# Optimization experiments

Measured on AMD Instinct MI355X. Metric: run time of the kernel, lower is better.

The kernel has to match this reference:

```python
import jax, jax.numpy as jnp
import numpy as np

N_NODES = 100000
N_EDGES = 1600000
IN_C, HID, OUT_C = 128, 64, 64
N_LAYERS = 16
ALPHA, THETA = 0.1, 0.5


def setup_inputs() -> dict:
    key = jax.random.key(0)
    ks = jax.random.split(key, 8)
    x = jax.random.normal(ks[0], (N_NODES, IN_C), dtype=jnp.float32)
    edge_index = jax.random.randint(ks[1], (2, N_EDGES), 0, N_NODES, dtype=jnp.int64)
    # torch Linear: weight [out, in], bias [out]
    lin0_w = jax.random.normal(ks[2], (HID, IN_C), dtype=jnp.float32) / np.sqrt(IN_C)
    lin0_b = jnp.zeros((HID,), dtype=jnp.float32)
    lin1_w = jax.random.normal(ks[3], (OUT_C, HID), dtype=jnp.float32) / np.sqrt(HID)
    lin1_b = jnp.zeros((OUT_C,), dtype=jnp.float32)
    # GCN2Conv weight1 per layer: [HID, HID], applied as h @ W
    conv_w = jax.random.normal(ks[4], (N_LAYERS, HID, HID), dtype=jnp.float32) / np.sqrt(HID)
    return {"x": x, "edge_index": edge_index, "lin0_w": lin0_w, "lin0_b": lin0_b,
            "lin1_w": lin1_w, "lin1_b": lin1_b, "conv_w": conv_w}


def reference(x, edge_index, lin0_w, lin0_b, lin1_w, lin1_b, conv_w):
    src, dst = edge_index[0], edge_index[1]
    # input projection (dropout p=0 in eval -> identity)
    h = jax.nn.relu(x @ lin0_w.T + lin0_b)  # [N, HID]
    h0 = h
    for l in range(N_LAYERS):
        # unweighted sum aggregation over edges (normalize=False, edge_weight=None)
        agg = jax.ops.segment_sum(h[src], dst, num_segments=N_NODES)  # [N, HID]
        z = (1.0 - ALPHA) * agg + ALPHA * h0  # initial residual
        beta = np.log(THETA / (l + 1) + 1.0).astype(np.float32)  # identity mapping strength
        h = jax.nn.relu((1.0 - beta) * z + beta * (z @ conv_w[l]))
    return h @ lin1_w.T + lin1_b  # [N, OUT_C]
```

## Files before the change

kernel.cpp:

```cpp
#include <hip/hip_runtime.h>
#include <cmath>

#define HID 64
#define IN_C 128

__device__ __forceinline__ float rl(float v, int k) {
    return __uint_as_float(__builtin_amdgcn_readlane(__float_as_uint(v), k));
}
__device__ __forceinline__ float bflo(unsigned u) { return __uint_as_float(u << 16); }
__device__ __forceinline__ float bfhi(unsigned u) { return __uint_as_float(u & 0xffff0000u); }
__device__ __forceinline__ unsigned bfpack(float lo, float hi) {
    unsigned a = __float_as_uint(lo), b = __float_as_uint(hi);
    a = (a + 0x7fffu + ((a >> 16) & 1u)) >> 16;
    b = (b + 0x7fffu + ((b >> 16) & 1u)) & 0xffff0000u;
    return a | b;
}


__global__ void k_hist(const int* __restrict__ dst, int* __restrict__ counts, int E) {
    int e = blockIdx.x * blockDim.x + threadIdx.x;
    if (e < E) atomicAdd(&counts[dst[e]], 1);
}

__global__ void k_scan_block(const int* __restrict__ counts, int* __restrict__ row_ptr,
                             int* __restrict__ chunk_sums, int n) {
    __shared__ int s[1024];
    int i = blockIdx.x * 1024 + threadIdx.x;
    int v = (i < n) ? counts[i] : 0;
    s[threadIdx.x] = v;
    __syncthreads();
    for (int off = 1; off < 1024; off <<= 1) {
        int t = (threadIdx.x >= off) ? s[threadIdx.x - off] : 0;
        __syncthreads();
        s[threadIdx.x] += t;
        __syncthreads();
    }
    if (i < n) row_ptr[i] = s[threadIdx.x] - v;
    if (threadIdx.x == 1023) chunk_sums[blockIdx.x] = s[1023];
}

__global__ void k_scan_fix(int* __restrict__ row_ptr, const int* __restrict__ chunk_sums,
                           int n, int total) {
    __shared__ int base_s;
    if (threadIdx.x == 0) {
        int b = 0;
        for (int c = 0; c < (int)blockIdx.x; ++c) b += chunk_sums[c];
        base_s = b;
    }
    __syncthreads();
    int i = blockIdx.x * 1024 + threadIdx.x;
    if (i < n) row_ptr[i] += base_s;
    if (i == 0) row_ptr[n] = total;
}

__global__ void k_fill(const int* __restrict__ src, const int* __restrict__ dst,
                       const int* __restrict__ row_ptr, int* __restrict__ cursor,
                       int* __restrict__ col_idx, int E) {
    int e = blockIdx.x * blockDim.x + threadIdx.x;
    if (e < E) {
        int d = dst[e];
        int pos = row_ptr[d] + atomicAdd(&cursor[d], 1);
        col_idx[pos] = src[e];
    }
}

__global__ __launch_bounds__(256) void k_lin0(const float* __restrict__ x,
                                              const float* __restrict__ w,
                                              const float* __restrict__ b,
                                              unsigned* __restrict__ h0, int N) {
    __shared__ float Wt[IN_C * 65];
    for (int i = threadIdx.x; i < IN_C * HID; i += 256) {
        int o = i >> 7, k = i & 127;
        Wt[k * 65 + o] = w[i];
    }
    __syncthreads();
    int lane = threadIdx.x & 63;
    int wid = (blockIdx.x * blockDim.x + threadIdx.x) >> 6;
    int nw = (gridDim.x * blockDim.x) >> 6;
    float bias = b[lane];
    for (int n0 = wid; n0 < N; n0 += 2 * nw) {
        int n1 = n0 + nw;
        bool v1 = n1 < N;
        int n1c = v1 ? n1 : n0;
        float xa0 = x[(size_t)n0 * IN_C + lane];
        float xa1 = x[(size_t)n0 * IN_C + 64 + lane];
        float xb0 = x[(size_t)n1c * IN_C + lane];
        float xb1 = x[(size_t)n1c * IN_C + 64 + lane];
        float acc0 = bias, acc1 = bias;
#pragma unroll
        for (int k = 0; k < 64; ++k) {
            float wv = Wt[k * 65 + lane];
            acc0 = fmaf(rl(xa0, k), wv, acc0);
            acc1 = fmaf(rl(xb0, k), wv, acc1);
        }
#pragma unroll
        for (int k = 0; k < 64; ++k) {
            float wv = Wt[(64 + k) * 65 + lane];
            acc0 = fmaf(rl(xa1, k), wv, acc0);
            acc1 = fmaf(rl(xb1, k), wv, acc1);
        }
        acc0 = fmaxf(acc0, 0.f);
        acc1 = fmaxf(acc1, 0.f);
        float p0 = __shfl(acc0, lane | 1);
        float p1 = __shfl(acc1, lane | 1);
        if ((lane & 1) == 0) {
            h0[(size_t)n0 * 32 + (lane >> 1)] = bfpack(acc0, p0);
            if (v1) h0[(size_t)n1 * 32 + (lane >> 1)] = bfpack(acc1, p1);
        }
    }
}

__global__ __launch_bounds__(256) void k_layer(const uint4* __restrict__ hin,
                                               const uint4* __restrict__ h0,
                                               unsigned* __restrict__ hout,
                                               const float* __restrict__ W,
                                               const int* __restrict__ row_ptr,
                                               const int* __restrict__ col_idx,
                                               float beta, int N) {
    __shared__ float Ws[HID * HID];
    for (int i = threadIdx.x; i < HID * HID; i += 256) Ws[i] = W[i];
    __syncthreads();

    int lane = threadIdx.x & 63;
    int sub = lane >> 3;
    int cg = lane & 7;
    int wid = (blockIdx.x * blockDim.x + threadIdx.x) >> 6;
    int nw = (gridDim.x * blockDim.x) >> 6;

    for (int n = wid; n < N; n += nw) {
        int b = row_ptr[n];
        int d = row_ptr[n + 1] - b;
        float a[8];
#pragma unroll
        for (int c = 0; c < 8; ++c) a[c] = 0.f;
        int j = 0;
        for (; j + 16 <= d; j += 16) {
            int i0 = col_idx[b + j + sub];
            int i1 = col_idx[b + j + 8 + sub];
            uint4 q0 = hin[(size_t)i0 * 8 + cg];
            uint4 q1 = hin[(size_t)i1 * 8 + cg];
            a[0] += bflo(q0.x); a[1] += bfhi(q0.x);
            a[2] += bflo(q0.y); a[3] += bfhi(q0.y);
            a[4] += bflo(q0.z); a[5] += bfhi(q0.z);
            a[6] += bflo(q0.w); a[7] += bfhi(q0.w);
            a[0] += bflo(q1.x); a[1] += bfhi(q1.x);
            a[2] += bflo(q1.y); a[3] += bfhi(q1.y);
            a[4] += bflo(q1.z); a[5] += bfhi(q1.z);
            a[6] += bflo(q1.w); a[7] += bfhi(q1.w);
        }
        if (j + sub < d) {
            int i0 = col_idx[b + j + sub];
            uint4 q0 = hin[(size_t)i0 * 8 + cg];
            a[0] += bflo(q0.x); a[1] += bfhi(q0.x);
            a[2] += bflo(q0.y); a[3] += bfhi(q0.y);
            a[4] += bflo(q0.z); a[5] += bfhi(q0.z);
            a[6] += bflo(q0.w); a[7] += bfhi(q0.w);
        }
        if (j + 8 + sub < d) {
            int i1 = col_idx[b + j + 8 + sub];
            uint4 q1 = hin[(size_t)i1 * 8 + cg];
            a[0] += bflo(q1.x); a[1] += bfhi(q1.x);
            a[2] += bflo(q1.y); a[3] += bfhi(q1.y);
            a[4] += bflo(q1.z); a[5] += bfhi(q1.z);
            a[6] += bflo(q1.w); a[7] += bfhi(q1.w);
        }
#pragma unroll
        for (int off = 8; off <= 32; off <<= 1) {
#pragma unroll
            for (int c = 0; c < 8; ++c) a[c] += __shfl_xor(a[c], off);
        }
        uint4 hq = h0[(size_t)n * 8 + cg];
        float z[8];
        z[0] = 0.9f * a[0] + 0.1f * bflo(hq.x);
        z[1] = 0.9f * a[1] + 0.1f * bfhi(hq.x);
        z[2] = 0.9f * a[2] + 0.1f * bflo(hq.y);
        z[3] = 0.9f * a[3] + 0.1f * bfhi(hq.y);
        z[4] = 0.9f * a[4] + 0.1f * bflo(hq.z);
        z[5] = 0.9f * a[5] + 0.1f * bfhi(hq.z);
        z[6] = 0.9f * a[6] + 0.1f * bflo(hq.w);
        z[7] = 0.9f * a[7] + 0.1f * bfhi(hq.w);

        float g = 0.f;
#pragma unroll
        for (int c = 0; c < 8; ++c) {
#pragma unroll
            for (int gg = 0; gg < 8; ++gg) {
                g = fmaf(rl(z[c], gg), Ws[(8 * gg + c) * HID + lane], g);
            }
        }
        int q = lane >> 3;
        float zs[8];
#pragma unroll
        for (int c = 0; c < 8; ++c) zs[c] = __shfl(z[c], q);
        int m = lane & 7;
        float zl = zs[0];
#pragma unroll
        for (int c = 1; c < 8; ++c) zl = (m == c) ? zs[c] : zl;

        float r = fmaxf((1.f - beta) * zl + beta * g, 0.f);
        float rn = __shfl(r, lane | 1);
        if ((lane & 1) == 0) hout[(size_t)n * 32 + (lane >> 1)] = bfpack(r, rn);
    }
}

__global__ __launch_bounds__(256) void k_lin1(const unsigned* __restrict__ h,
                                              const float* __restrict__ w,
                                              const float* __restrict__ b,
                                              float* __restrict__ out, int N) {
    __shared__ float Wt[HID * 65];
    for (int i = threadIdx.x; i < HID * HID; i += 256) {
        int o = i >> 6, k = i & 63;
        Wt[k * 65 + o] = w[i];
    }
    __syncthreads();
    int lane = threadIdx.x & 63;
    int wid = (blockIdx.x * blockDim.x + threadIdx.x) >> 6;
    int nw = (gridDim.x * blockDim.x) >> 6;
    float bias = b[lane];
    for (int n0 = wid; n0 < N; n0 += 2 * nw) {
        int n1 = n0 + nw;
        bool v1 = n1 < N;
        int n1c = v1 ? n1 : n0;
        unsigned ua = h[(size_t)n0 * 32 + (lane >> 1)];
        unsigned ub = h[(size_t)n1c * 32 + (lane >> 1)];
        float ha = (lane & 1) ? bfhi(ua) : bflo(ua);
        float hb = (lane & 1) ? bfhi(ub) : bflo(ub);
        float acc0 = bias, acc1 = bias;
#pragma unroll
        for (int k = 0; k < 64; ++k) {
            float wv = Wt[k * 65 + lane];
            acc0 = fmaf(rl(ha, k), wv, acc0);
            acc1 = fmaf(rl(hb, k), wv, acc1);
        }
        out[(size_t)n0 * HID + lane] = acc0;
        if (v1) out[(size_t)n1 * HID + lane] = acc1;
    }
}

extern "C" void kernel_launch(void* const* d_in, const int* in_sizes, int n_in,
                              void* d_out, int out_size, void* d_ws, size_t ws_size,
                              hipStream_t stream) {
    const float* x      = (const float*)d_in[0];
    const int*   ei     = (const int*)d_in[1];
    const float* lin0_w = (const float*)d_in[2];
    const float* lin0_b = (const float*)d_in[3];
    const float* lin1_w = (const float*)d_in[4];
    const float* lin1_b = (const float*)d_in[5];
    const float* conv_w = (const float*)d_in[6];

    int N = in_sizes[0] / IN_C;
    int E = in_sizes[1] / 2;
    const int* src = ei;
    const int* dst = ei + E;

    unsigned* h0 = (unsigned*)d_ws;
    unsigned* hA = h0 + (size_t)N * 32;
    unsigned* hB = hA + (size_t)N * 32;
    int* row_ptr    = (int*)(hB + (size_t)N * 32);
    int* cursor     = row_ptr + (N + 1);
    int* col_idx    = cursor + N;
    int* chunk_sums = col_idx + E;

    int nch = (N + 1023) / 1024;

    hipMemsetAsync(cursor, 0, (size_t)N * sizeof(int), stream);
    k_hist<<<(E + 255) / 256, 256, 0, stream>>>(dst, cursor, E);
    k_scan_block<<<nch, 1024, 0, stream>>>(cursor, row_ptr, chunk_sums, N);
    k_scan_fix<<<nch, 1024, 0, stream>>>(row_ptr, chunk_sums, N, E);
    hipMemsetAsync(cursor, 0, (size_t)N * sizeof(int), stream);
    k_fill<<<(E + 255) / 256, 256, 0, stream>>>(src, dst, row_ptr, cursor, col_idx, E);

    k_lin0<<<1024, 256, 0, stream>>>(x, lin0_w, lin0_b, h0, N);

    const unsigned* cur = h0;
    for (int l = 0; l < 16; ++l) {
        float beta = (float)log(0.5 / (double)(l + 1) + 1.0);
        unsigned* nxt = (l & 1) ? hB : hA;
        k_layer<<<2048, 256, 0, stream>>>((const uint4*)cur, (const uint4*)h0, nxt,
                                          conv_w + (size_t)l * HID * HID,
                                          row_ptr, col_idx, beta, N);
        cur = nxt;
    }

    k_lin1<<<1024, 256, 0, stream>>>(cur, lin1_w, lin1_b, (float*)d_out, N);
}
```

Baseline: 1.478 ms.

## Use DPP/permlane reductions, bf16-packed LDS weights and LDS z broadcast in layer kernel

After: 1.511 ms. 1.02x slower.

```diff
diff --git a/kernel.cpp b/kernel.cpp
--- a/kernel.cpp
+++ b/kernel.cpp
@@ -14,6 +14,33 @@
     a = (a + 0x7fffu + ((a >> 16) & 1u)) >> 16;
     b = (b + 0x7fffu + ((b >> 16) & 1u)) & 0xffff0000u;
     return a | b;
+}
+
+__device__ __forceinline__ float xadd8(float x) {
+    int t = __builtin_amdgcn_update_dpp(0, __float_as_int(x), 0x128, 0xF, 0xF, true);
+    return x + __int_as_float(t);
+}
+#if __has_builtin(__builtin_amdgcn_permlane16_swap)
+typedef unsigned uvec2 __attribute__((ext_vector_type(2)));
+__device__ __forceinline__ float xadd16(float x) {
+    uvec2 r = __builtin_amdgcn_permlane16_swap(__float_as_uint(x), __float_as_uint(x), false, false);
+    return __uint_as_float(r[0]) + __uint_as_float(r[1]);
+}
+#else
+__device__ __forceinline__ float xadd16(float x) { return x + __shfl_xor(x, 16); }
+#endif
+#if __has_builtin(__builtin_amdgcn_permlane32_swap)
+typedef unsigned uvec2b __attribute__((ext_vector_type(2)));
+__device__ __forceinline__ float xadd32(float x) {
+    uvec2b r = __builtin_amdgcn_permlane32_swap(__float_as_uint(x), __float_as_uint(x), false, false);
+    return __uint_as_float(r[0]) + __uint_as_float(r[1]);
+}
+#else
+__device__ __forceinline__ float xadd32(float x) { return x + __shfl_xor(x, 32); }
+#endif
+__device__ __forceinline__ float pairswap(float x) {
+    int t = __builtin_amdgcn_update_dpp(0, __float_as_int(x), 0xB1, 0xF, 0xF, true);
+    return __int_as_float(t);
 }
 
 
@@ -101,8 +128,8 @@
         }
         acc0 = fmaxf(acc0, 0.f);
         acc1 = fmaxf(acc1, 0.f);
-        float p0 = __shfl(acc0, lane | 1);
-        float p1 = __shfl(acc1, lane | 1);
+        float p0 = pairswap(acc0);
+        float p1 = pairswap(acc1);
         if ((lane & 1) == 0) {
             h0[(size_t)n0 * 32 + (lane >> 1)] = bfpack(acc0, p0);
             if (v1) h0[(size_t)n1 * 32 + (lane >> 1)] = bfpack(acc1, p1);
@@ -117,11 +144,23 @@
                                                const int* __restrict__ row_ptr,
                                                const int* __restrict__ col_idx,
                                                float beta, int N) {
-    __shared__ float Ws[HID * HID];
-    for (int i = threadIdx.x; i < HID * HID; i += 256) Ws[i] = W[i];
+    __shared__ uint2 Wp[16 * 64];
+    __shared__ float zb[4 * 64];
+    for (int idx = threadIdx.x; idx < 16 * 64; idx += 256) {
+        int k4 = idx >> 6, c = idx & 63;
+        float w0 = W[(4 * k4 + 0) * 64 + c];
+        float w1 = W[(4 * k4 + 1) * 64 + c];
+        float w2 = W[(4 * k4 + 2) * 64 + c];
+        float w3 = W[(4 * k4 + 3) * 64 + c];
+        uint2 p;
+        p.x = bfpack(w0, w1);
+        p.y = bfpack(w2, w3);
+        Wp[idx] = p;
+    }
     __syncthreads();
 
     int lane = threadIdx.x & 63;
+    int wslot = threadIdx.x >> 6;
     int sub = lane >> 3;
     int cg = lane & 7;
     int wid = (blockIdx.x * blockDim.x + threadIdx.x) >> 6;
@@ -165,10 +204,12 @@
             a[6] += bflo(q1.w); a[7] += bfhi(q1.w);
         }
 #pragma unroll
-        for (int off = 8; off <= 32; off <<= 1) {
-#pragma unroll
-            for (int c = 0; c < 8; ++c) a[c] += __shfl_xor(a[c], off);
-        }
+        for (int c = 0; c < 8; ++c) a[c] = xadd8(a[c]);
+#pragma unroll
+        for (int c = 0; c < 8; ++c) a[c] = xadd16(a[c]);
+#pragma unroll
+        for (int c = 0; c < 8; ++c) a[c] = xadd32(a[c]);
+
         uint4 hq = h0[(size_t)n * 8 + cg];
         float z[8];
         z[0] = 0.9f * a[0] + 0.1f * bflo(hq.x);
@@ -180,25 +221,28 @@
         z[6] = 0.9f * a[6] + 0.1f * bflo(hq.w);
         z[7] = 0.9f * a[7] + 0.1f * bfhi(hq.w);
 
-        float g = 0.f;
-#pragma unroll
-        for (int c = 0; c < 8; ++c) {
-#pragma unroll
-            for (int gg = 0; gg < 8; ++gg) {
-                g = fmaf(rl(z[c], gg), Ws[(8 * gg + c) * HID + lane], g);
-            }
-        }
-        int q = lane >> 3;
-        float zs[8];
-#pragma unroll
-        for (int c = 0; c < 8; ++c) zs[c] = __shfl(z[c], q);
-        int m = lane & 7;
-        float zl = zs[0];
-#pragma unroll
-        for (int c = 1; c < 8; ++c) zl = (m == c) ? zs[c] : zl;
+        if (sub == 0) {
+            float4 zlo = make_float4(z[0], z[1], z[2], z[3]);
+            float4 zhi = make_float4(z[4], z[5], z[6], z[7]);
+            *(float4*)&zb[wslot * 64 + cg * 8]     = zlo;
+            *(float4*)&zb[wslot * 64 + cg * 8 + 4] = zhi;
+        }
+        float zl = zb[wslot * 64 + lane];
+
+        float g0 = 0.f, g1 = 0.f, g2 = 0.f, g3 = 0.f;
+#pragma unroll
+        for (int k4 = 0; k4 < 16; ++k4) {
+            uint2 wp = Wp[k4 * 64 + lane];
+            int k = 4 * k4;
+            g0 = fmaf(rl(z[(k + 0) & 7], (k + 0) >> 3), bflo(wp.x), g0);
+            g1 = fmaf(rl(z[(k + 1) & 7], (k + 1) >> 3), bfhi(wp.x), g1);
+            g2 = fmaf(rl(z[(k + 2) & 7], (k + 2) >> 3), bflo(wp.y), g2);
+            g3 = fmaf(rl(z[(k + 3) & 7], (k + 3) >> 3), bfhi(wp.y), g3);
+        }
+        float g = (g0 + g1) + (g2 + g3);
 
         float r = fmaxf((1.f - beta) * zl + beta * g, 0.f);
-        float rn = __shfl(r, lane | 1);
+        float rn = pairswap(r);
         if ((lane & 1) == 0) hout[(size_t)n * 32 + (lane >> 1)] = bfpack(r, rn);
     }
 }
```
